# Performance work log

Hardware: AMD Instinct MI355X
Metric: run time of the kernel (lower is better)

Reference implementation:

```python
import jax, jax.numpy as jnp
import numpy as np

NUM_HEADS = 8
DEPTH_K = 256
DEPTH_V = 256


def rel_to_abs(x):
    # x: [B, Nh, L, 2L-1] -> [B, Nh, L, L] via the pad/reshape skew trick
    B, Nh, L, _ = x.shape
    x = jnp.pad(x, ((0, 0), (0, 0), (0, 0), (0, 1)))            # [B,Nh,L,2L]
    flat = x.reshape(B, Nh, L * 2 * L)
    flat = jnp.pad(flat, ((0, 0), (0, 0), (0, L - 1)))
    final = flat.reshape(B, Nh, L + 1, 2 * L - 1)
    return final[:, :, :L, L - 1:]


def relative_logits_1d(q, rel_k, H, W, transpose_mask):
    # q: [B, Nh, H, W, d]; rel_k: [2W-1, d]
    B, Nh = q.shape[0], q.shape[1]
    rel = jnp.einsum('bhxyd,md->bhxym', q, rel_k)               # [B,Nh,H,W,2W-1]
    rel = rel.reshape(B, Nh * H, W, 2 * W - 1)
    rel = rel_to_abs(rel)                                       # [B,Nh*H,W,W]
    rel = rel.reshape(B, Nh, H, W, W)
    rel = jnp.broadcast_to(rel[:, :, :, None, :, :], (B, Nh, H, H, W, W))
    rel = jnp.transpose(rel, transpose_mask)
    return rel.reshape(B, Nh, H * W, H * W)


def split_heads_2d(x):
    B, H, W, c = x.shape
    x = x.reshape(B, H, W, NUM_HEADS, c // NUM_HEADS)
    return jnp.transpose(x, (0, 3, 1, 2, 4))                     # [B,Nh,H,W,d]


def setup_inputs() -> dict:
    key = jax.random.key(0)
    k1, k2, k3 = jax.random.split(key, 3)
    dk_head = DEPTH_K // NUM_HEADS
    H = W = 32
    inputs = jax.random.normal(k1, (8, H, W, 2 * DEPTH_K + DEPTH_V), dtype=jnp.float32)
    key_rel_w = jax.random.normal(k2, (2 * W - 1, dk_head), dtype=jnp.float32) * dk_head ** -0.5
    key_rel_h = jax.random.normal(k3, (2 * H - 1, dk_head), dtype=jnp.float32) * dk_head ** -0.5
    return {"inputs": inputs, "key_rel_w": key_rel_w, "key_rel_h": key_rel_h}


def reference(inputs, key_rel_w, key_rel_h):
    B, H, W, _ = inputs.shape
    q, k, v = jnp.split(inputs, [DEPTH_K, 2 * DEPTH_K], axis=-1)
    q = split_heads_2d(q) * (DEPTH_K / NUM_HEADS) ** -0.5        # [B,Nh,H,W,dk]
    k = split_heads_2d(k)
    v = split_heads_2d(v)

    flat_q = q.reshape(B, NUM_HEADS, H * W, -1)
    flat_k = k.reshape(B, NUM_HEADS, H * W, -1)
    flat_v = v.reshape(B, NUM_HEADS, H * W, -1)

    logits = jnp.einsum('bnqd,bnkd->bnqk', flat_q, flat_k)       # [B,Nh,HW,HW]
    w_rel = relative_logits_1d(q, key_rel_w, H, W, (0, 1, 2, 4, 3, 5))
    h_rel = relative_logits_1d(jnp.transpose(q, (0, 1, 3, 2, 4)), key_rel_h,
                               W, H, (0, 1, 4, 2, 5, 3))
    logits = logits + h_rel + w_rel

    weights = jax.nn.softmax(logits, axis=-1)
    attn = jnp.einsum('bnqk,bnkd->bnqd', weights, flat_v)        # [B,Nh,HW,dv]
    attn = attn.reshape(B, NUM_HEADS, H, W, -1)
    out = jnp.transpose(attn, (0, 2, 3, 1, 4)).reshape(B, H, W, DEPTH_V)
    return out
```

## Files before the change

### kernel.cpp

```cpp
#include <hip/hip_runtime.h>
#include <hip/hip_bf16.h>

typedef short bf16x8 __attribute__((ext_vector_type(8)));
typedef float f32x4  __attribute__((ext_vector_type(4)));
typedef unsigned uintx2 __attribute__((ext_vector_type(2)));

#define DEVINL static __device__ __forceinline__

DEVINL unsigned short f2bf(float x){
  union { float f; unsigned u; } v; v.f = x;
  unsigned r = v.u + 0x7fffu + ((v.u >> 16) & 1u);
  return (unsigned short)(r >> 16);
}
DEVINL float bf2f(unsigned short b){
  union { unsigned u; float f; } v; v.u = ((unsigned)b) << 16; return v.f;
}
DEVINL unsigned pk2(float a, float b){
  __hip_bfloat162 h = __float22bfloat162_rn(float2{a, b});
  union { __hip_bfloat162 h2; unsigned u; } cv; cv.h2 = h; return cv.u;
}
DEVINL float fexp2(float x){
  float r; asm("v_exp_f32 %0, %1" : "=v"(r) : "v"(x)); return r;
}

__global__ __launch_bounds__(512, 4)
void aug_attn_kernel(const float* __restrict__ inp,
                     const float* __restrict__ relw,
                     const float* __restrict__ relh,
                     float* __restrict__ out)
{
  __shared__ __align__(16) unsigned short s_rw[128*66];
  __shared__ __align__(16) unsigned short s_rh[128*34];
  __shared__ __align__(16) unsigned short s_k [2][64*40];
  __shared__ __align__(16) unsigned short s_vt[2][32*64];

  const int tid  = threadIdx.x;
  const int wv   = tid >> 6;
  const int lane = tid & 63;
  const int lo16 = lane & 15;
  const int hi4  = lane >> 4;

  const int bid = blockIdx.x;
  const int bn  = bid >> 3;
  const int qc  = bid & 7;
  const int b   = bn >> 3;
  const int n   = bn & 7;
  const int x1l = wv >> 1;
  const int qh  = wv & 1;
  const int x1  = qc*4 + x1l;
  const int y1  = qh*16 + lo16;
  const int qrow = x1l*32 + y1;

  const float qscale = 0.17677669529663687f;
  const float L2E    = 1.44269504088896f;
  const float MFIX   = 8.0f;

  const int krow = tid >> 3;
  const int c4   = (tid & 7) << 2;
  const float* kptr = inp + ((size_t)(b*1024 + krow))*768 + 256 + n*32 + c4;
  const float* vptr = kptr + 256;
  const size_t kstep = (size_t)64*768;

  float4 kA = *(const float4*)kptr;
  float4 vA = *(const float4*)vptr;

  int vslot[4];
#pragma unroll
  for (int j=0;j<4;++j){
    const int dv = c4 + j;
    vslot[j] = dv*64 + ((((krow>>3) ^ (dv&7) ^ ((dv>>3)&3)))<<3) + (krow&7);
  }

  bf16x8 qf;
  {
    const float* qp = inp + ((size_t)((b*32 + x1)*32 + y1))*768 + n*32 + hi4*8;
    float4 a = *(const float4*)qp;
    float4 c = *(const float4*)(qp+4);
    union { unsigned u[4]; bf16x8 v; } cv;
    cv.u[0]=pk2(a.x*qscale, a.y*qscale);
    cv.u[1]=pk2(a.z*qscale, a.w*qscale);
    cv.u[2]=pk2(c.x*qscale, c.y*qscale);
    cv.u[3]=pk2(c.z*qscale, c.w*qscale);
    qf = cv.v;
  }

#pragma unroll
  for (int mt=0; mt<4; ++mt){
    const int m = mt*16 + lo16;
    bf16x8 rf = {0,0,0,0,0,0,0,0};
    if (m < 63){
      const float* rp = relw + m*32 + hi4*8;
      float4 a = *(const float4*)rp;
      float4 c = *(const float4*)(rp+4);
      union { unsigned u[4]; bf16x8 v; } cv;
      cv.u[0]=pk2(a.x,a.y); cv.u[1]=pk2(a.z,a.w);
      cv.u[2]=pk2(c.x,c.y); cv.u[3]=pk2(c.z,c.w);
      rf = cv.v;
    }
    f32x4 acc = {0.f,0.f,0.f,0.f};
    acc = __builtin_amdgcn_mfma_f32_16x16x32_bf16(qf, rf, acc, 0,0,0);
    const int rw0 = x1l*32 + qh*16 + hi4*4;
#pragma unroll
    for (int r=0;r<4;++r)
      s_rw[(rw0+r)*66 + m] = f2bf(acc[r]);
  }

#pragma unroll
  for (int mt=0; mt<4; ++mt){
    const int m = mt*16 + lo16;
    bf16x8 rf = {0,0,0,0,0,0,0,0};
    if (m < 63){
      const float* rp = relh + m*32 + hi4*8;
      float4 a = *(const float4*)rp;
      float4 c = *(const float4*)(rp+4);
      union { unsigned u[4]; bf16x8 v; } cv;
      cv.u[0]=pk2(a.x,a.y); cv.u[1]=pk2(a.z,a.w);
      cv.u[2]=pk2(c.x,c.y); cv.u[3]=pk2(c.z,c.w);
      rf = cv.v;
    }
    const int x2 = m + x1 - 31;
    f32x4 acc = {0.f,0.f,0.f,0.f};
    acc = __builtin_amdgcn_mfma_f32_16x16x32_bf16(qf, rf, acc, 0,0,0);
    if (x2 >= 0 && x2 < 32){
      const int rw0 = x1l*32 + qh*16 + hi4*4;
#pragma unroll
      for (int r=0;r<4;++r)
        s_rh[(rw0+r)*34 + x2] = f2bf(acc[r]);
    }
  }

  float rwl2[2][4];
  {
    const int mb = 31 - y1 + 4*hi4;
#pragma unroll
    for (int p=0;p<2;++p)
#pragma unroll
      for (int r=0;r<4;++r)
        rwl2[p][r] = (bf2f(s_rw[qrow*66 + mb + 16*p + r]) - MFIX)*L2E;
  }

  float l_run = 0.f;
  f32x4 accO[2];
  {
    f32x4 z = {0.f,0.f,0.f,0.f};
    accO[0] = z; accO[1] = z;
  }

  for (int kb=0; kb<16; ++kb){
    const int cur = kb & 1;
    {
      uintx2 kw; kw[0]=pk2(kA.x,kA.y); kw[1]=pk2(kA.z,kA.w);
      *(uintx2*)(&s_k[cur][krow*40 + c4]) = kw;
      const unsigned u0 = pk2(vA.x, vA.y), u1 = pk2(vA.z, vA.w);
      unsigned short* vt = s_vt[cur];
      vt[vslot[0]] = (unsigned short)u0;
      vt[vslot[1]] = (unsigned short)(u0>>16);
      vt[vslot[2]] = (unsigned short)u1;
      vt[vslot[3]] = (unsigned short)(u1>>16);
    }
    __syncthreads();

    if (kb < 15){
      kptr += kstep; vptr += kstep;
      kA = *(const float4*)kptr;
      vA = *(const float4*)vptr;
    }

    bf16x8 kfrag[4];
#pragma unroll
    for (int kt=0;kt<4;++kt)
      kfrag[kt] = *(const bf16x8*)(&s_k[cur][(kt*16 + lo16)*40 + hi4*8]);

    bf16x8 vfrag[2][2];
#pragma unroll
    for (int dvt=0;dvt<2;++dvt){
      const int dv = dvt*16 + lo16;
      const int xr = (dv&7) ^ ((dv>>3)&3);
#pragma unroll
      for (int kc=0;kc<2;++kc){
        const int blk = (kc*4 + hi4) ^ xr;
        vfrag[dvt][kc] = *(const bf16x8*)(&s_vt[cur][dv*64 + blk*8]);
      }
    }

    f32x4 S[4];
#pragma unroll
    for (int kt=0;kt<4;++kt){
      f32x4 z = {0.f,0.f,0.f,0.f};
      S[kt] = __builtin_amdgcn_mfma_f32_16x16x32_bf16(kfrag[kt], qf, z, 0,0,0);
    }

    const unsigned rhu = *(const unsigned*)(&s_rh[qrow*34 + 2*kb]);
    const float rh0L = bf2f((unsigned short)(rhu & 0xffffu))*L2E;
    const float rh1L = bf2f((unsigned short)(rhu >> 16))*L2E;
    unsigned W[4][2];
    float lacc = 0.f;
#pragma unroll
    for (int kt=0;kt<4;++kt){
      const float rhL = (kt<2)? rh0L : rh1L;
      const int p = kt & 1;
      float pv0 = fexp2(__builtin_fmaf(S[kt][0], L2E, rwl2[p][0] + rhL));
      float pv1 = fexp2(__builtin_fmaf(S[kt][1], L2E, rwl2[p][1] + rhL));
      float pv2 = fexp2(__builtin_fmaf(S[kt][2], L2E, rwl2[p][2] + rhL));
      float pv3 = fexp2(__builtin_fmaf(S[kt][3], L2E, rwl2[p][3] + rhL));
      lacc += (pv0+pv1) + (pv2+pv3);
      W[kt][0] = pk2(pv0, pv1);
      W[kt][1] = pk2(pv2, pv3);
    }
    l_run += lacc;

    bf16x8 pfrag[2];
#pragma unroll
    for (int kc=0;kc<2;++kc){
      unsigned r0 = W[2*kc][0],   r1 = W[2*kc][1];
      unsigned r2 = W[2*kc+1][0], r3 = W[2*kc+1][1];
      asm("v_permlane32_swap_b32 %0, %1" : "+v"(r0), "+v"(r2));
      asm("v_permlane32_swap_b32 %0, %1" : "+v"(r1), "+v"(r3));
      asm("v_permlane16_swap_b32 %0, %1" : "+v"(r0), "+v"(r2));
      asm("v_permlane16_swap_b32 %0, %1" : "+v"(r1), "+v"(r3));
      union { unsigned u[4]; bf16x8 v; } cv;
      cv.u[0]=r0; cv.u[1]=r1; cv.u[2]=r2; cv.u[3]=r3;
      pfrag[kc] = cv.v;
    }

#pragma unroll
    for (int kc=0;kc<2;++kc)
#pragma unroll
      for (int dvt=0;dvt<2;++dvt)
        accO[dvt] = __builtin_amdgcn_mfma_f32_16x16x32_bf16(
                      vfrag[dvt][kc], pfrag[kc], accO[dvt], 0,0,0);
  }

  float l = l_run;
  l += __shfl_xor(l, 16, 64);
  l += __shfl_xor(l, 32, 64);
  const float inv = 1.f / l;
  float* op = out + ((size_t)((b*32 + x1)*32 + y1))*256 + n*32;
#pragma unroll
  for (int dvt=0;dvt<2;++dvt){
    float4 o;
    o.x = accO[dvt][0]*inv;
    o.y = accO[dvt][1]*inv;
    o.z = accO[dvt][2]*inv;
    o.w = accO[dvt][3]*inv;
    *(float4*)(op + dvt*16 + hi4*4) = o;
  }
}

extern "C" void kernel_launch(void* const* d_in, const int* in_sizes, int n_in,
                              void* d_out, int out_size, void* d_ws, size_t ws_size,
                              hipStream_t stream) {
  (void)in_sizes; (void)n_in; (void)d_ws; (void)ws_size; (void)out_size;
  const float* inp  = (const float*)d_in[0];
  const float* relw = (const float*)d_in[1];
  const float* relh = (const float*)d_in[2];
  float* out = (float*)d_out;
  dim3 grid(512), block(512);
  aug_attn_kernel<<<grid, block, 0, stream>>>(inp, relw, relh, out);
}
```

Before: 102.1 us.

## Stage 128 keys per barrier and add MFMA priority hints

Each loop phase now loads and stages 128 key/value rows (two 64-row sub-tiles) instead of 64, with 8 floats per thread, which halves the number of block barriers and widens the global loads and LDS stores. The plain __syncthreads is replaced by an explicit lgkmcnt wait plus s_barrier, and s_setprio raises wave priority around the MFMA groups. LDS use doubles and more registers hold prefetched data, which may reduce occupancy.

```diff
diff --git a/kernel.cpp b/kernel.cpp
--- a/kernel.cpp
+++ b/kernel.cpp
@@ -3,7 +3,6 @@
 
 typedef short bf16x8 __attribute__((ext_vector_type(8)));
 typedef float f32x4  __attribute__((ext_vector_type(4)));
-typedef unsigned uintx2 __attribute__((ext_vector_type(2)));
 
 #define DEVINL static __device__ __forceinline__
 
@@ -31,8 +30,8 @@
 {
   __shared__ __align__(16) unsigned short s_rw[128*66];
   __shared__ __align__(16) unsigned short s_rh[128*34];
-  __shared__ __align__(16) unsigned short s_k [2][64*40];
-  __shared__ __align__(16) unsigned short s_vt[2][32*64];
+  __shared__ __align__(16) unsigned short s_k [2][128*40];
+  __shared__ __align__(16) unsigned short s_vt[2][4096];
 
   const int tid  = threadIdx.x;
   const int wv   = tid >> 6;
@@ -55,20 +54,23 @@
   const float L2E    = 1.44269504088896f;
   const float MFIX   = 8.0f;
 
-  const int krow = tid >> 3;
-  const int c4   = (tid & 7) << 2;
-  const float* kptr = inp + ((size_t)(b*1024 + krow))*768 + 256 + n*32 + c4;
+  const int krow = tid >> 2;
+  const int c8   = (tid & 3) * 8;
+  const float* kptr = inp + ((size_t)(b*1024 + krow))*768 + 256 + n*32 + c8;
   const float* vptr = kptr + 256;
-  const size_t kstep = (size_t)64*768;
+  const size_t kstep = (size_t)128*768;
 
   float4 kA = *(const float4*)kptr;
+  float4 kB = *(const float4*)(kptr+4);
   float4 vA = *(const float4*)vptr;
-
-  int vslot[4];
-#pragma unroll
-  for (int j=0;j<4;++j){
-    const int dv = c4 + j;
-    vslot[j] = dv*64 + ((((krow>>3) ^ (dv&7) ^ ((dv>>3)&3)))<<3) + (krow&7);
+  float4 vB = *(const float4*)(vptr+4);
+
+  const int vst = krow >> 6, vkr = krow & 63;
+  int vslot[8];
+#pragma unroll
+  for (int j=0;j<8;++j){
+    const int dv = c8 + j;
+    vslot[j] = vst*2048 + dv*64 + (((vkr>>3) ^ (dv&7) ^ ((dv>>3)&3))<<3) + (vkr&7);
   }
 
   bf16x8 qf;
@@ -146,89 +148,99 @@
     accO[0] = z; accO[1] = z;
   }
 
-  for (int kb=0; kb<16; ++kb){
-    const int cur = kb & 1;
+  for (int ph=0; ph<8; ++ph){
+    const int cur = ph & 1;
     {
-      uintx2 kw; kw[0]=pk2(kA.x,kA.y); kw[1]=pk2(kA.z,kA.w);
-      *(uintx2*)(&s_k[cur][krow*40 + c4]) = kw;
-      const unsigned u0 = pk2(vA.x, vA.y), u1 = pk2(vA.z, vA.w);
+      uint4 kw; kw.x=pk2(kA.x,kA.y); kw.y=pk2(kA.z,kA.w);
+                kw.z=pk2(kB.x,kB.y); kw.w=pk2(kB.z,kB.w);
+      *(uint4*)(&s_k[cur][krow*40 + c8]) = kw;
+      const unsigned u0=pk2(vA.x,vA.y), u1=pk2(vA.z,vA.w);
+      const unsigned u2=pk2(vB.x,vB.y), u3=pk2(vB.z,vB.w);
       unsigned short* vt = s_vt[cur];
-      vt[vslot[0]] = (unsigned short)u0;
-      vt[vslot[1]] = (unsigned short)(u0>>16);
-      vt[vslot[2]] = (unsigned short)u1;
-      vt[vslot[3]] = (unsigned short)(u1>>16);
-    }
-    __syncthreads();
-
-    if (kb < 15){
+      vt[vslot[0]]=(unsigned short)u0;  vt[vslot[1]]=(unsigned short)(u0>>16);
+      vt[vslot[2]]=(unsigned short)u1;  vt[vslot[3]]=(unsigned short)(u1>>16);
+      vt[vslot[4]]=(unsigned short)u2;  vt[vslot[5]]=(unsigned short)(u2>>16);
+      vt[vslot[6]]=(unsigned short)u3;  vt[vslot[7]]=(unsigned short)(u3>>16);
+    }
+    asm volatile("s_waitcnt lgkmcnt(0)" ::: "memory");
+    __builtin_amdgcn_s_barrier();
+    asm volatile("" ::: "memory");
+
+    if (ph < 7){
       kptr += kstep; vptr += kstep;
-      kA = *(const float4*)kptr;
-      vA = *(const float4*)vptr;
-    }
-
-    bf16x8 kfrag[4];
-#pragma unroll
-    for (int kt=0;kt<4;++kt)
-      kfrag[kt] = *(const bf16x8*)(&s_k[cur][(kt*16 + lo16)*40 + hi4*8]);
-
-    bf16x8 vfrag[2][2];
-#pragma unroll
-    for (int dvt=0;dvt<2;++dvt){
-      const int dv = dvt*16 + lo16;
-      const int xr = (dv&7) ^ ((dv>>3)&3);
+      kA = *(const float4*)kptr; kB = *(const float4*)(kptr+4);
+      vA = *(const float4*)vptr; vB = *(const float4*)(vptr+4);
+    }
+
+#pragma unroll
+    for (int st=0; st<2; ++st){
+      bf16x8 kfrag[4];
+#pragma unroll
+      for (int kt=0;kt<4;++kt)
+        kfrag[kt] = *(const bf16x8*)(&s_k[cur][(st*64 + kt*16 + lo16)*40 + hi4*8]);
+      bf16x8 vfrag[2][2];
+#pragma unroll
+      for (int dvt=0;dvt<2;++dvt){
+        const int dv = dvt*16 + lo16;
+        const int xr = (dv&7) ^ ((dv>>3)&3);
+#pragma unroll
+        for (int kc=0;kc<2;++kc){
+          const int blk = (kc*4 + hi4) ^ xr;
+          vfrag[dvt][kc] = *(const bf16x8*)(&s_vt[cur][st*2048 + dv*64 + blk*8]);
+        }
+      }
+
+      f32x4 S[4];
+      __builtin_amdgcn_s_setprio(1);
+#pragma unroll
+      for (int kt=0;kt<4;++kt){
+        f32x4 z = {0.f,0.f,0.f,0.f};
+        S[kt] = __builtin_amdgcn_mfma_f32_16x16x32_bf16(kfrag[kt], qf, z, 0,0,0);
+      }
+      __builtin_amdgcn_s_setprio(0);
+
+      const unsigned rhu = *(const unsigned*)(&s_rh[qrow*34 + 4*ph + 2*st]);
+      const float rh0L = bf2f((unsigned short)(rhu & 0xffffu))*L2E;
+      const float rh1L = bf2f((unsigned short)(rhu >> 16))*L2E;
+      unsigned W[4][2];
+      float lacc = 0.f;
+#pragma unroll
+      for (int kt=0;kt<4;++kt){
+        const float rhL = (kt<2)? rh0L : rh1L;
+        const int p = kt & 1;
+        float pv0 = fexp2(__builtin_fmaf(S[kt][0], L2E, rwl2[p][0] + rhL));
+        float pv1 = fexp2(__builtin_fmaf(S[kt][1], L2E, rwl2[p][1] + rhL));
+        float pv2 = fexp2(__builtin_fmaf(S[kt][2], L2E, rwl2[p][2] + rhL));
+        float pv3 = fexp2(__builtin_fmaf(S[kt][3], L2E, rwl2[p][3] + rhL));
+        lacc += (pv0+pv1) + (pv2+pv3);
+        W[kt][0] = pk2(pv0, pv1);
+        W[kt][1] = pk2(pv2, pv3);
+      }
+      l_run += lacc;
+
+      bf16x8 pfrag[2];
 #pragma unroll
       for (int kc=0;kc<2;++kc){
-        const int blk = (kc*4 + hi4) ^ xr;
-        vfrag[dvt][kc] = *(const bf16x8*)(&s_vt[cur][dv*64 + blk*8]);
-      }
-    }
-
-    f32x4 S[4];
-#pragma unroll
-    for (int kt=0;kt<4;++kt){
-      f32x4 z = {0.f,0.f,0.f,0.f};
-      S[kt] = __builtin_amdgcn_mfma_f32_16x16x32_bf16(kfrag[kt], qf, z, 0,0,0);
-    }
-
-    const unsigned rhu = *(const unsigned*)(&s_rh[qrow*34 + 2*kb]);
-    const float rh0L = bf2f((unsigned short)(rhu & 0xffffu))*L2E;
-    const float rh1L = bf2f((unsigned short)(rhu >> 16))*L2E;
-    unsigned W[4][2];
-    float lacc = 0.f;
-#pragma unroll
-    for (int kt=0;kt<4;++kt){
-      const float rhL = (kt<2)? rh0L : rh1L;
-      const int p = kt & 1;
-      float pv0 = fexp2(__builtin_fmaf(S[kt][0], L2E, rwl2[p][0] + rhL));
-      float pv1 = fexp2(__builtin_fmaf(S[kt][1], L2E, rwl2[p][1] + rhL));
-      float pv2 = fexp2(__builtin_fmaf(S[kt][2], L2E, rwl2[p][2] + rhL));
-      float pv3 = fexp2(__builtin_fmaf(S[kt][3], L2E, rwl2[p][3] + rhL));
-      lacc += (pv0+pv1) + (pv2+pv3);
-      W[kt][0] = pk2(pv0, pv1);
-      W[kt][1] = pk2(pv2, pv3);
-    }
-    l_run += lacc;
-
-    bf16x8 pfrag[2];
-#pragma unroll
-    for (int kc=0;kc<2;++kc){
-      unsigned r0 = W[2*kc][0],   r1 = W[2*kc][1];
-      unsigned r2 = W[2*kc+1][0], r3 = W[2*kc+1][1];
-      asm("v_permlane32_swap_b32 %0, %1" : "+v"(r0), "+v"(r2));
-      asm("v_permlane32_swap_b32 %0, %1" : "+v"(r1), "+v"(r3));
-      asm("v_permlane16_swap_b32 %0, %1" : "+v"(r0), "+v"(r2));
-      asm("v_permlane16_swap_b32 %0, %1" : "+v"(r1), "+v"(r3));
-      union { unsigned u[4]; bf16x8 v; } cv;
-      cv.u[0]=r0; cv.u[1]=r1; cv.u[2]=r2; cv.u[3]=r3;
-      pfrag[kc] = cv.v;
-    }
-
-#pragma unroll
-    for (int kc=0;kc<2;++kc)
-#pragma unroll
-      for (int dvt=0;dvt<2;++dvt)
-        accO[dvt] = __builtin_amdgcn_mfma_f32_16x16x32_bf16(
-                      vfrag[dvt][kc], pfrag[kc], accO[dvt], 0,0,0);
+        unsigned r0 = W[2*kc][0],   r1 = W[2*kc][1];
+        unsigned r2 = W[2*kc+1][0], r3 = W[2*kc+1][1];
+        asm("v_permlane32_swap_b32 %0, %1" : "+v"(r0), "+v"(r2));
+        asm("v_permlane32_swap_b32 %0, %1" : "+v"(r1), "+v"(r3));
+        asm("v_permlane16_swap_b32 %0, %1" : "+v"(r0), "+v"(r2));
+        asm("v_permlane16_swap_b32 %0, %1" : "+v"(r1), "+v"(r3));
+        union { unsigned u[4]; bf16x8 v; } cv;
+        cv.u[0]=r0; cv.u[1]=r1; cv.u[2]=r2; cv.u[3]=r3;
+        pfrag[kc] = cv.v;
+      }
+
+      __builtin_amdgcn_s_setprio(1);
+#pragma unroll
+      for (int kc=0;kc<2;++kc)
+#pragma unroll
+        for (int dvt=0;dvt<2;++dvt)
+          accO[dvt] = __builtin_amdgcn_mfma_f32_16x16x32_bf16(
+                        vfrag[dvt][kc], pfrag[kc], accO[dvt], 0,0,0);
+      __builtin_amdgcn_s_setprio(0);
+    }
   }
 
   float l = l_run;
```

Result: no change. 100.7 us (-1.3%).
